# Kernel tuning notes

Measured on AMD Instinct MI355X. Metric: run time of the kernel, lower is better.

Reference implementation:

```python
import jax, jax.numpy as jnp
import numpy as np

N_EMBD = 1024
HEAD_SIZE = 64


def setup_inputs() -> dict:
    key = jax.random.key(0)
    kx, kq, kk, kv = jax.random.split(key, 4)
    B, T = 8, 2048
    x = jax.random.normal(kx, (B, T, N_EMBD), dtype=jnp.float32)
    s = 1.0 / np.sqrt(N_EMBD)
    Wq = jax.random.normal(kq, (N_EMBD, HEAD_SIZE), dtype=jnp.float32) * s
    Wk = jax.random.normal(kk, (N_EMBD, HEAD_SIZE), dtype=jnp.float32) * s
    Wv = jax.random.normal(kv, (N_EMBD, HEAD_SIZE), dtype=jnp.float32) * s
    return {"x": x, "Wq": Wq, "Wk": Wk, "Wv": Wv}


def reference(x, Wq, Wk, Wv):
    # x: [B, T, C]; W*: [C, H]
    q = jnp.einsum('btc,ch->bth', x, Wq)
    k = jnp.einsum('btc,ch->bth', x, Wk)
    v = jnp.einsum('btc,ch->bth', x, Wv)
    H = q.shape[-1]
    score = jnp.einsum('bth,bsh->bts', q, k) / jnp.sqrt(jnp.asarray(H, q.dtype))
    T = score.shape[-1]
    causal = jnp.tril(jnp.ones((T, T), dtype=bool))  # [T, T]
    score = jnp.where(causal, score, -jnp.inf)
    attn = jax.nn.softmax(score, axis=-1)
    return jnp.einsum('bts,bsh->bth', attn, v)
```

## Files before the change

kernel.cpp:

```cpp
#include <hip/hip_runtime.h>

typedef __bf16 bf16;
typedef __attribute__((ext_vector_type(8))) __bf16 bf16x8;
typedef __attribute__((ext_vector_type(4))) __bf16 bf16x4;
typedef __attribute__((ext_vector_type(4))) float floatx4;

#define MFMA16(a, b, c) __builtin_amdgcn_mfma_f32_16x16x32_bf16((a), (b), (c), 0, 0, 0)

__global__ void prep_w(const float* __restrict__ Wq, const float* __restrict__ Wk,
                       const float* __restrict__ Wv, bf16* __restrict__ wTf) {
    int tid = blockIdx.x * 256 + threadIdx.x;
    int j = tid & 7;
    int l = (tid >> 3) & 15;
    int q = (tid >> 7) & 3;
    int kc = (tid >> 9) & 31;
    int mt = tid >> 14;
    int mat = mt >> 2;
    int h = ((mt & 3) << 4) + l;
    int c = kc * 32 + q * 8 + j;
    const float* W = (mat == 0) ? Wq : (mat == 1) ? Wk : Wv;
    wTf[tid] = (bf16)W[c * 64 + h];
}

__global__ __launch_bounds__(256, 2) void proj_qkv(const float* __restrict__ x,
                                                   const bf16* __restrict__ wTf,
                                                   bf16* __restrict__ q,
                                                   bf16* __restrict__ k,
                                                   bf16* __restrict__ vT) {
    __shared__ __align__(16) char xsb[32 * 2048];

    const int tid = threadIdx.x;
    const int lane = tid & 63;
    const int w = tid >> 6;
    const int l15 = lane & 15;
    const int quad = lane >> 4;
    const int T0 = blockIdx.x * 32;

    const int r = tid >> 4;
    const int cm = tid & 15;
    const float* g0 = x + (size_t)(T0 + r) * 1024 + cm * 8;
    const float* g1 = x + (size_t)(T0 + r + 16) * 1024 + cm * 8;
    char* ld0 = xsb + r * 2048;
    char* ld1 = xsb + (r + 16) * 2048;
    const int sws = (r & 7) << 4;

#define STC8(ldb, c, f0, f1)                                                    \
    {                                                                            \
        bf16x8 pk;                                                               \
        pk[0] = (bf16)(f0)[0]; pk[1] = (bf16)(f0)[1];                            \
        pk[2] = (bf16)(f0)[2]; pk[3] = (bf16)(f0)[3];                            \
        pk[4] = (bf16)(f1)[0]; pk[5] = (bf16)(f1)[1];                            \
        pk[6] = (bf16)(f1)[2]; pk[7] = (bf16)(f1)[3];                            \
        *(bf16x8*)((ldb) + ((cm * 16 + (c) * 256) ^ sws)) = pk;                  \
    }

    floatx4 fA[8], fB[8], hA[8], hB[8];
    #pragma unroll
    for (int c = 0; c < 4; c++) {
        fA[2*c]   = *(const floatx4*)(g0 + c * 128);
        fA[2*c+1] = *(const floatx4*)(g0 + c * 128 + 4);
        fB[2*c]   = *(const floatx4*)(g1 + c * 128);
        fB[2*c+1] = *(const floatx4*)(g1 + c * 128 + 4);
    }
    #pragma unroll
    for (int c = 0; c < 4; c++) {
        hA[2*c]   = *(const floatx4*)(g0 + 512 + c * 128);
        hA[2*c+1] = *(const floatx4*)(g0 + 512 + c * 128 + 4);
        hB[2*c]   = *(const floatx4*)(g1 + 512 + c * 128);
        hB[2*c+1] = *(const floatx4*)(g1 + 512 + c * 128 + 4);
    }
    #pragma unroll
    for (int c = 0; c < 4; c++) {
        STC8(ld0, c, fA[2*c], fA[2*c+1]);
        STC8(ld1, c, fB[2*c], fB[2*c+1]);
    }
    __syncthreads();

    floatx4 acc[6] = {};
    const bf16* aw0 = wTf + (size_t)(w * 3 + 0) * 16384 + lane * 8;
    const bf16* aw1 = wTf + (size_t)(w * 3 + 1) * 16384 + lane * 8;
    const bf16* aw2 = wTf + (size_t)(w * 3 + 2) * 16384 + lane * 8;
    const char* xr = xsb + l15 * 2048;
    const int sx = (l15 & 7) << 4;
    const int q16 = quad * 16;

    bf16x8 a0c = *(const bf16x8*)(aw0);
    bf16x8 a1c = *(const bf16x8*)(aw1);
    bf16x8 a2c = *(const bf16x8*)(aw2);
    bf16x8 a0n = *(const bf16x8*)(aw0 + 512);
    bf16x8 a1n = *(const bf16x8*)(aw1 + 512);
    bf16x8 a2n = *(const bf16x8*)(aw2 + 512);

#define KBODY(kc)                                                               \
    {                                                                            \
        bf16x8 p0 = *(const bf16x8*)(aw0 + ((kc) + 2) * 512);                    \
        bf16x8 p1 = *(const bf16x8*)(aw1 + ((kc) + 2) * 512);                    \
        bf16x8 p2 = *(const bf16x8*)(aw2 + ((kc) + 2) * 512);                    \
        const int o = ((kc) * 64 + q16) ^ sx;                                    \
        bf16x8 b0 = *(const bf16x8*)(xr + o);                                    \
        bf16x8 b1 = *(const bf16x8*)(xr + 32768 + o);                            \
        acc[0] = MFMA16(a0c, b0, acc[0]);                                        \
        acc[1] = MFMA16(a0c, b1, acc[1]);                                        \
        acc[2] = MFMA16(a1c, b0, acc[2]);                                        \
        acc[3] = MFMA16(a1c, b1, acc[3]);                                        \
        acc[4] = MFMA16(a2c, b0, acc[4]);                                        \
        acc[5] = MFMA16(a2c, b1, acc[5]);                                        \
        a0c = a0n; a1c = a1n; a2c = a2n;                                         \
        a0n = p0;  a1n = p1;  a2n = p2;                                          \
    }

    #pragma unroll 4
    for (int kc = 0; kc < 16; kc++) KBODY(kc);

    #pragma unroll
    for (int c = 4; c < 8; c++) {
        STC8(ld0, c, hA[2*(c-4)], hA[2*(c-4)+1]);
        STC8(ld1, c, hB[2*(c-4)], hB[2*(c-4)+1]);
    }
    __syncthreads();

    #pragma unroll 4
    for (int kc = 16; kc < 32; kc++) KBODY(kc);
#undef KBODY
#undef STC8

    #pragma unroll
    for (int i = 0; i < 3; i++) {
        int mtile = w * 3 + i;
        int mat = mtile >> 2;
        int hbase = ((mtile & 3) << 4) + (quad << 2);
        float sc = (mat == 0) ? 0.18033688011112042f : 1.0f;
        #pragma unroll
        for (int tt = 0; tt < 2; tt++) {
            const int t = T0 + tt * 16 + l15;
            floatx4 av = acc[i * 2 + tt];
            bf16x4 pk;
            pk[0] = (bf16)(av[0] * sc);
            pk[1] = (bf16)(av[1] * sc);
            pk[2] = (bf16)(av[2] * sc);
            pk[3] = (bf16)(av[3] * sc);
            if (mat == 0) {
                *(bf16x4*)(q + (size_t)t * 64 + hbase) = pk;
            } else if (mat == 1) {
                *(bf16x4*)(k + (size_t)t * 64 + hbase) = pk;
            } else {
                int bidx = t >> 11, tmod = t & 2047;
                #pragma unroll
                for (int rr = 0; rr < 4; rr++)
                    vT[(size_t)(bidx * 64 + hbase + rr) * 2048 + tmod] = pk[rr];
            }
        }
    }
}

#define KP2 72
#define OH 68

__global__ __launch_bounds__(512, 4) void flash(const bf16* __restrict__ q,
                                                const bf16* __restrict__ k,
                                                const bf16* __restrict__ vT,
                                                float* __restrict__ out) {
    __shared__ char smem[8 * 16 * OH * 4];
    __shared__ float Ms[8][16], Ls[8][16];
    bf16* psall = (bf16*)smem;
    float* Os = (float*)smem;

    const int b = blockIdx.x & 7;
    const int p = blockIdx.x >> 3;
    const int t0A = p * 16;
    const int t0B = (127 - p) * 16;
    const int nttA = (p >> 2) + 1;
    const int nttB = ((127 - p) >> 2) + 1;
    const int L = nttA + nttB;

    const int tid = threadIdx.x;
    const int w = tid >> 6;
    const int lane = tid & 63;
    const int l15 = lane & 15;
    const int quad = lane >> 4;

    const int s0 = (L * w) >> 3;
    const int s1 = (L * (w + 1)) >> 3;

    const bf16* kbase = k + (size_t)(b * 2048 + l15) * 64 + quad * 8;
    const bf16* vbase = vT + (size_t)(b * 64 + l15) * 2048 + quad * 8;
    bf16* psw = psall + w * 16 * KP2;

    const bf16* qpA = q + (size_t)(b * 2048 + t0A + l15) * 64 + quad * 8;
    const bf16* qpB = q + (size_t)(b * 2048 + t0B + l15) * 64 + quad * 8;

    floatx4 oA[4] = {}, oB[4] = {};
    float miA = -1e30f, liA = 0.f, miB = -1e30f, liB = 0.f;

#define KV_STEP(jtv, isdiag, t0v, qf0v, qf1v, mi_, li_, o_)                          \
    {                                                                                 \
        const bf16* kp = kbase + (size_t)(jtv) * 4096;                                \
        floatx4 stt[4];                                                               \
        __builtin_amdgcn_s_setprio(1);                                                \
        _Pragma("unroll") for (int mt = 0; mt < 4; mt++) {                            \
            floatx4 z = {};                                                           \
            bf16x8 ka0 = *(const bf16x8*)(kp + mt * 1024);                            \
            bf16x8 ka1 = *(const bf16x8*)(kp + mt * 1024 + 32);                       \
            z = MFMA16(ka0, qf0v, z);                                                 \
            z = MFMA16(ka1, qf1v, z);                                                 \
            stt[mt] = z;                                                              \
        }                                                                             \
        __builtin_amdgcn_s_setprio(0);                                                \
        if (isdiag) {                                                                 \
            _Pragma("unroll") for (int mt = 0; mt < 4; mt++)                          \
                _Pragma("unroll") for (int rr = 0; rr < 4; rr++) {                    \
                    int kv = (jtv) * 64 + mt * 16 + quad * 4 + rr;                    \
                    if (kv > (t0v) + l15) stt[mt][rr] = -1e30f;                       \
                }                                                                     \
        }                                                                             \
        float m0_ = fmaxf(fmaxf(stt[0][0], stt[0][1]), stt[0][2]);                    \
        float m1_ = fmaxf(fmaxf(stt[0][3], stt[1][0]), stt[1][1]);                    \
        float m2_ = fmaxf(fmaxf(stt[1][2], stt[1][3]), stt[2][0]);                    \
        float m3_ = fmaxf(fmaxf(stt[2][1], stt[2][2]), stt[2][3]);                    \
        float m4_ = fmaxf(fmaxf(stt[3][0], stt[3][1]), stt[3][2]);                    \
        float mx = fmaxf(fmaxf(fmaxf(m0_, m1_), m2_),                                 \
                         fmaxf(fmaxf(m3_, m4_), stt[3][3]));                          \
        mx = fmaxf(mx, __shfl_xor(mx, 16, 64));                                       \
        mx = fmaxf(mx, __shfl_xor(mx, 32, 64));                                       \
        const bool nodefer = !__all(mx - mi_ <= 8.0f);                                \
        const float mnew = nodefer ? fmaxf(mi_, mx) : mi_;                            \
        float rs = 0.f;                                                               \
        _Pragma("unroll") for (int mt = 0; mt < 4; mt++)                              \
            _Pragma("unroll") for (int rr = 0; rr < 4; rr++) {                        \
                float pv = __builtin_amdgcn_exp2f(stt[mt][rr] - mnew);                \
                stt[mt][rr] = pv;                                                     \
                rs += pv;                                                             \
            }                                                                         \
        rs += __shfl_xor(rs, 16, 64);                                                 \
        rs += __shfl_xor(rs, 32, 64);                                                 \
        if (nodefer) {                                                                \
            const float aa = __builtin_amdgcn_exp2f(mi_ - mnew);                      \
            mi_ = mnew;                                                               \
            li_ *= aa;                                                                \
            _Pragma("unroll") for (int mt = 0; mt < 4; mt++)                          \
                _Pragma("unroll") for (int rr = 0; rr < 4; rr++) o_[mt][rr] *= aa;    \
        }                                                                             \
        li_ += rs;                                                                    \
        _Pragma("unroll") for (int mt = 0; mt < 4; mt++) {                            \
            bf16x4 pk;                                                                \
            pk[0] = (bf16)stt[mt][0]; pk[1] = (bf16)stt[mt][1];                       \
            pk[2] = (bf16)stt[mt][2]; pk[3] = (bf16)stt[mt][3];                       \
            *(bf16x4*)(psw + l15 * KP2 + mt * 16 + quad * 4) = pk;                    \
        }                                                                             \
        const bf16* vp = vbase + (jtv) * 64;                                          \
        __builtin_amdgcn_s_setprio(1);                                                \
        _Pragma("unroll") for (int kc = 0; kc < 2; kc++) {                            \
            bf16x8 pb = *(const bf16x8*)(psw + l15 * KP2 + kc * 32 + quad * 8);       \
            _Pragma("unroll") for (int mt = 0; mt < 4; mt++) {                        \
                bf16x8 va = *(const bf16x8*)(vp + mt * 32768 + kc * 32);              \
                o_[mt] = MFMA16(va, pb, o_[mt]);                                      \
            }                                                                         \
        }                                                                             \
        __builtin_amdgcn_s_setprio(0);                                                \
    }

    {
        const int eA = (s1 < nttA) ? s1 : nttA;
        if (s0 < eA) {
            bf16x8 qf0 = *(const bf16x8*)qpA;
            bf16x8 qf1 = *(const bf16x8*)(qpA + 32);
            for (int s = s0; s < eA; s++) {
                KV_STEP(s, (s == nttA - 1), t0A, qf0, qf1, miA, liA, oA);
            }
        }
    }
    {
        const int sB = (s0 > nttA) ? s0 : nttA;
        if (sB < s1) {
            bf16x8 qf0 = *(const bf16x8*)qpB;
            bf16x8 qf1 = *(const bf16x8*)(qpB + 32);
            for (int s = sB; s < s1; s++) {
                KV_STEP(s - nttA, (s == L - 1), t0B, qf0, qf1, miB, liB, oB);
            }
        }
    }

    #pragma unroll
    for (int tile = 0; tile < 2; tile++) {
        __syncthreads();
        float mi = tile ? miB : miA;
        float li = tile ? liB : liA;
        if (lane < 16) { Ms[w][lane] = mi; Ls[w][lane] = li; }
        #pragma unroll
        for (int mt = 0; mt < 4; mt++) {
            floatx4 ov = tile ? oB[mt] : oA[mt];
            *(floatx4*)(Os + (w * 16 + l15) * OH + mt * 16 + quad * 4) = ov;
        }
        __syncthreads();
        {
            int qq = tid >> 5;
            int h2 = (tid & 31) * 2;
            float Mg = -1e30f;
            #pragma unroll
            for (int u = 0; u < 8; u++) Mg = fmaxf(Mg, Ms[u][qq]);
            float Lg = 0.f, v0 = 0.f, v1 = 0.f;
            #pragma unroll
            for (int u = 0; u < 8; u++) {
                float sw = __builtin_amdgcn_exp2f(Ms[u][qq] - Mg);
                Lg += sw * Ls[u][qq];
                const float* Or = Os + (u * 16 + qq) * OH + h2;
                v0 += sw * Or[0];
                v1 += sw * Or[1];
            }
            float inv = 1.0f / Lg;
            int t0v = tile ? t0B : t0A;
            float* op = out + (size_t)(b * 2048 + t0v + qq) * 64 + h2;
            op[0] = v0 * inv;
            op[1] = v1 * inv;
        }
    }
#undef KV_STEP
}

extern "C" void kernel_launch(void* const* d_in, const int* in_sizes, int n_in,
                              void* d_out, int out_size, void* d_ws, size_t ws_size,
                              hipStream_t stream) {
    const float* x  = (const float*)d_in[0];
    const float* Wq = (const float*)d_in[1];
    const float* Wk = (const float*)d_in[2];
    const float* Wv = (const float*)d_in[3];
    float* out = (float*)d_out;

    char* ws = (char*)d_ws;
    bf16* wTf = (bf16*)ws;
    bf16* q   = (bf16*)(ws + 397312);
    bf16* k   = (bf16*)(ws + 397312 + 2097152);
    bf16* vT  = (bf16*)(ws + 397312 + 2 * 2097152);

    hipLaunchKernelGGL(prep_w,   dim3(768), dim3(256), 0, stream, Wq, Wk, Wv, wTf);
    hipLaunchKernelGGL(proj_qkv, dim3(512), dim3(256), 0, stream, x, wTf, q, k, vT);
    hipLaunchKernelGGL(flash,    dim3(512), dim3(512), 0, stream, q, k, vT, out);
}
```

Baseline: 140.5 us.

## Process two query tiles per KV step in flash kernel to reuse K/V loads

Each flash block now handles four 16-row query tiles (two near, two far) instead of two. Each wave loads a K and V tile once and feeds it to two query tiles, which halves K/V global loads per unit of work. The grid drops to 256 blocks and launch bounds drop to 2 blocks per SM to make room for the extra registers and shared memory. Costs are higher register pressure, fewer blocks to hide latency, and coarser load balancing, since the diagonal mask now covers two tiles that share the same KV range.

```diff
diff --git a/kernel.cpp b/kernel.cpp
--- a/kernel.cpp
+++ b/kernel.cpp
@@ -155,23 +155,26 @@
 
 #define KP2 72
 #define OH 68
-
-__global__ __launch_bounds__(512, 4) void flash(const bf16* __restrict__ q,
+#define PSB (16 * KP2)
+
+__global__ __launch_bounds__(512, 2) void flash(const bf16* __restrict__ q,
                                                 const bf16* __restrict__ k,
                                                 const bf16* __restrict__ vT,
                                                 float* __restrict__ out) {
-    __shared__ char smem[8 * 16 * OH * 4];
+    __shared__ char smem[36864];
     __shared__ float Ms[8][16], Ls[8][16];
     bf16* psall = (bf16*)smem;
     float* Os = (float*)smem;
 
     const int b = blockIdx.x & 7;
-    const int p = blockIdx.x >> 3;
-    const int t0A = p * 16;
-    const int t0B = (127 - p) * 16;
-    const int nttA = (p >> 2) + 1;
-    const int nttB = ((127 - p) >> 2) + 1;
-    const int L = nttA + nttB;
+    const int j = blockIdx.x >> 3;
+    const int Tn0 = 32 * j;
+    const int Tn1 = Tn0 + 16;
+    const int Tf0 = (126 - 2 * j) * 16;
+    const int Tf1 = Tf0 + 16;
+    const int NN = (j >> 1) + 1;
+    const int NF = ((63 - j) >> 1) + 1;
+    const int L = NN + NF;
 
     const int tid = threadIdx.x;
     const int w = tid >> 6;
@@ -179,116 +182,155 @@
     const int l15 = lane & 15;
     const int quad = lane >> 4;
 
-    const int s0 = (L * w) >> 3;
-    const int s1 = (L * (w + 1)) >> 3;
+    const int u0 = (L * w) >> 3;
+    const int u1 = (L * (w + 1)) >> 3;
 
     const bf16* kbase = k + (size_t)(b * 2048 + l15) * 64 + quad * 8;
     const bf16* vbase = vT + (size_t)(b * 64 + l15) * 2048 + quad * 8;
-    bf16* psw = psall + w * 16 * KP2;
-
-    const bf16* qpA = q + (size_t)(b * 2048 + t0A + l15) * 64 + quad * 8;
-    const bf16* qpB = q + (size_t)(b * 2048 + t0B + l15) * 64 + quad * 8;
-
-    floatx4 oA[4] = {}, oB[4] = {};
-    float miA = -1e30f, liA = 0.f, miB = -1e30f, liB = 0.f;
-
-#define KV_STEP(jtv, isdiag, t0v, qf0v, qf1v, mi_, li_, o_)                          \
+    bf16* pswa = psall + w * 2 * PSB;
+    bf16* pswb = pswa + PSB;
+
+    const bf16* qn0 = q + (size_t)(b * 2048 + Tn0 + l15) * 64 + quad * 8;
+    const bf16* qn1 = q + (size_t)(b * 2048 + Tn1 + l15) * 64 + quad * 8;
+    const bf16* qx0 = q + (size_t)(b * 2048 + Tf0 + l15) * 64 + quad * 8;
+    const bf16* qx1 = q + (size_t)(b * 2048 + Tf1 + l15) * 64 + quad * 8;
+
+    floatx4 o0[4] = {}, o1[4] = {}, o2[4] = {}, o3[4] = {};
+    float mm0 = -1e30f, ll0 = 0.f, mm1 = -1e30f, ll1 = 0.f;
+    float mm2 = -1e30f, ll2 = 0.f, mm3 = -1e30f, ll3 = 0.f;
+
+#define SMPART(mi_, li_, o_, pswX)                                                   \
     {                                                                                 \
-        const bf16* kp = kbase + (size_t)(jtv) * 4096;                                \
+        float x0_ = fmaxf(fmaxf(stt[0][0], stt[0][1]), stt[0][2]);                    \
+        float x1_ = fmaxf(fmaxf(stt[0][3], stt[1][0]), stt[1][1]);                    \
+        float x2_ = fmaxf(fmaxf(stt[1][2], stt[1][3]), stt[2][0]);                    \
+        float x3_ = fmaxf(fmaxf(stt[2][1], stt[2][2]), stt[2][3]);                    \
+        float x4_ = fmaxf(fmaxf(stt[3][0], stt[3][1]), stt[3][2]);                    \
+        float mx_ = fmaxf(fmaxf(fmaxf(x0_, x1_), x2_),                                \
+                          fmaxf(fmaxf(x3_, x4_), stt[3][3]));                         \
+        mx_ = fmaxf(mx_, __shfl_xor(mx_, 16, 64));                                    \
+        mx_ = fmaxf(mx_, __shfl_xor(mx_, 32, 64));                                    \
+        const bool nd_ = !__all(mx_ - mi_ <= 8.0f);                                   \
+        const float mn_ = nd_ ? fmaxf(mi_, mx_) : mi_;                                \
+        float rs_ = 0.f;                                                              \
+        _Pragma("unroll") for (int mt_ = 0; mt_ < 4; mt_++)                           \
+            _Pragma("unroll") for (int rr_ = 0; rr_ < 4; rr_++) {                     \
+                float pv_ = __builtin_amdgcn_exp2f(stt[mt_][rr_] - mn_);              \
+                stt[mt_][rr_] = pv_;                                                  \
+                rs_ += pv_;                                                           \
+            }                                                                         \
+        rs_ += __shfl_xor(rs_, 16, 64);                                               \
+        rs_ += __shfl_xor(rs_, 32, 64);                                               \
+        if (nd_) {                                                                    \
+            const float aa_ = __builtin_amdgcn_exp2f(mi_ - mn_);                      \
+            mi_ = mn_;                                                                \
+            li_ *= aa_;                                                               \
+            _Pragma("unroll") for (int mt_ = 0; mt_ < 4; mt_++)                       \
+                _Pragma("unroll") for (int rr_ = 0; rr_ < 4; rr_++) o_[mt_][rr_] *= aa_; \
+        }                                                                             \
+        li_ += rs_;                                                                   \
+        _Pragma("unroll") for (int mt_ = 0; mt_ < 4; mt_++) {                         \
+            bf16x4 pk_;                                                               \
+            pk_[0] = (bf16)stt[mt_][0]; pk_[1] = (bf16)stt[mt_][1];                   \
+            pk_[2] = (bf16)stt[mt_][2]; pk_[3] = (bf16)stt[mt_][3];                   \
+            *(bf16x4*)((pswX) + l15 * KP2 + mt_ * 16 + quad * 4) = pk_;               \
+        }                                                                             \
+    }
+
+#define KV_STEP2(jtv, isdiag, T0a_, T0b_, qa0_, qa1_, qb0_, qb1_,                     \
+                 m_a, l_a, o_a, m_b, l_b, o_b)                                        \
+    {                                                                                 \
+        const bf16* kp_ = kbase + (size_t)(jtv) * 4096;                               \
+        bf16x8 kv0_ = *(const bf16x8*)(kp_);                                          \
+        bf16x8 kv1_ = *(const bf16x8*)(kp_ + 32);                                     \
+        bf16x8 kv2_ = *(const bf16x8*)(kp_ + 1024);                                   \
+        bf16x8 kv3_ = *(const bf16x8*)(kp_ + 1024 + 32);                              \
+        bf16x8 kv4_ = *(const bf16x8*)(kp_ + 2048);                                   \
+        bf16x8 kv5_ = *(const bf16x8*)(kp_ + 2048 + 32);                              \
+        bf16x8 kv6_ = *(const bf16x8*)(kp_ + 3072);                                   \
+        bf16x8 kv7_ = *(const bf16x8*)(kp_ + 3072 + 32);                              \
         floatx4 stt[4];                                                               \
         __builtin_amdgcn_s_setprio(1);                                                \
-        _Pragma("unroll") for (int mt = 0; mt < 4; mt++) {                            \
-            floatx4 z = {};                                                           \
-            bf16x8 ka0 = *(const bf16x8*)(kp + mt * 1024);                            \
-            bf16x8 ka1 = *(const bf16x8*)(kp + mt * 1024 + 32);                       \
-            z = MFMA16(ka0, qf0v, z);                                                 \
-            z = MFMA16(ka1, qf1v, z);                                                 \
-            stt[mt] = z;                                                              \
-        }                                                                             \
+        { floatx4 z_ = {}; z_ = MFMA16(kv0_, qa0_, z_); z_ = MFMA16(kv1_, qa1_, z_); stt[0] = z_; } \
+        { floatx4 z_ = {}; z_ = MFMA16(kv2_, qa0_, z_); z_ = MFMA16(kv3_, qa1_, z_); stt[1] = z_; } \
+        { floatx4 z_ = {}; z_ = MFMA16(kv4_, qa0_, z_); z_ = MFMA16(kv5_, qa1_, z_); stt[2] = z_; } \
+        { floatx4 z_ = {}; z_ = MFMA16(kv6_, qa0_, z_); z_ = MFMA16(kv7_, qa1_, z_); stt[3] = z_; } \
         __builtin_amdgcn_s_setprio(0);                                                \
         if (isdiag) {                                                                 \
-            _Pragma("unroll") for (int mt = 0; mt < 4; mt++)                          \
-                _Pragma("unroll") for (int rr = 0; rr < 4; rr++) {                    \
-                    int kv = (jtv) * 64 + mt * 16 + quad * 4 + rr;                    \
-                    if (kv > (t0v) + l15) stt[mt][rr] = -1e30f;                       \
+            _Pragma("unroll") for (int mt_ = 0; mt_ < 4; mt_++)                       \
+                _Pragma("unroll") for (int rr_ = 0; rr_ < 4; rr_++) {                 \
+                    int kv_ = (jtv) * 64 + mt_ * 16 + quad * 4 + rr_;                 \
+                    if (kv_ > (T0a_) + l15) stt[mt_][rr_] = -1e30f;                   \
                 }                                                                     \
         }                                                                             \
-        float m0_ = fmaxf(fmaxf(stt[0][0], stt[0][1]), stt[0][2]);                    \
-        float m1_ = fmaxf(fmaxf(stt[0][3], stt[1][0]), stt[1][1]);                    \
-        float m2_ = fmaxf(fmaxf(stt[1][2], stt[1][3]), stt[2][0]);                    \
-        float m3_ = fmaxf(fmaxf(stt[2][1], stt[2][2]), stt[2][3]);                    \
-        float m4_ = fmaxf(fmaxf(stt[3][0], stt[3][1]), stt[3][2]);                    \
-        float mx = fmaxf(fmaxf(fmaxf(m0_, m1_), m2_),                                 \
-                         fmaxf(fmaxf(m3_, m4_), stt[3][3]));                          \
-        mx = fmaxf(mx, __shfl_xor(mx, 16, 64));                                       \
-        mx = fmaxf(mx, __shfl_xor(mx, 32, 64));                                       \
-        const bool nodefer = !__all(mx - mi_ <= 8.0f);                                \
-        const float mnew = nodefer ? fmaxf(mi_, mx) : mi_;                            \
-        float rs = 0.f;                                                               \
-        _Pragma("unroll") for (int mt = 0; mt < 4; mt++)                              \
-            _Pragma("unroll") for (int rr = 0; rr < 4; rr++) {                        \
-                float pv = __builtin_amdgcn_exp2f(stt[mt][rr] - mnew);                \
-                stt[mt][rr] = pv;                                                     \
-                rs += pv;                                                             \
-            }                                                                         \
-        rs += __shfl_xor(rs, 16, 64);                                                 \
-        rs += __shfl_xor(rs, 32, 64);                                                 \
-        if (nodefer) {                                                                \
-            const float aa = __builtin_amdgcn_exp2f(mi_ - mnew);                      \
-            mi_ = mnew;                                                               \
-            li_ *= aa;                                                                \
-            _Pragma("unroll") for (int mt = 0; mt < 4; mt++)                          \
-                _Pragma("unroll") for (int rr = 0; rr < 4; rr++) o_[mt][rr] *= aa;    \
-        }                                                                             \
-        li_ += rs;                                                                    \
-        _Pragma("unroll") for (int mt = 0; mt < 4; mt++) {                            \
-            bf16x4 pk;                                                                \
-            pk[0] = (bf16)stt[mt][0]; pk[1] = (bf16)stt[mt][1];                       \
-            pk[2] = (bf16)stt[mt][2]; pk[3] = (bf16)stt[mt][3];                       \
-            *(bf16x4*)(psw + l15 * KP2 + mt * 16 + quad * 4) = pk;                    \
-        }                                                                             \
-        const bf16* vp = vbase + (jtv) * 64;                                          \
+        SMPART(m_a, l_a, o_a, pswa);                                                  \
         __builtin_amdgcn_s_setprio(1);                                                \
-        _Pragma("unroll") for (int kc = 0; kc < 2; kc++) {                            \
-            bf16x8 pb = *(const bf16x8*)(psw + l15 * KP2 + kc * 32 + quad * 8);       \
-            _Pragma("unroll") for (int mt = 0; mt < 4; mt++) {                        \
-                bf16x8 va = *(const bf16x8*)(vp + mt * 32768 + kc * 32);              \
-                o_[mt] = MFMA16(va, pb, o_[mt]);                                      \
-            }                                                                         \
-        }                                                                             \
+        { floatx4 z_ = {}; z_ = MFMA16(kv0_, qb0_, z_); z_ = MFMA16(kv1_, qb1_, z_); stt[0] = z_; } \
+        { floatx4 z_ = {}; z_ = MFMA16(kv2_, qb0_, z_); z_ = MFMA16(kv3_, qb1_, z_); stt[1] = z_; } \
+        { floatx4 z_ = {}; z_ = MFMA16(kv4_, qb0_, z_); z_ = MFMA16(kv5_, qb1_, z_); stt[2] = z_; } \
+        { floatx4 z_ = {}; z_ = MFMA16(kv6_, qb0_, z_); z_ = MFMA16(kv7_, qb1_, z_); stt[3] = z_; } \
         __builtin_amdgcn_s_setprio(0);                                                \
+        if (isdiag) {                                                                 \
+            _Pragma("unroll") for (int mt_ = 0; mt_ < 4; mt_++)                       \
+                _Pragma("unroll") for (int rr_ = 0; rr_ < 4; rr_++) {                 \
+                    int kv_ = (jtv) * 64 + mt_ * 16 + quad * 4 + rr_;                 \
+                    if (kv_ > (T0b_) + l15) stt[mt_][rr_] = -1e30f;                   \
+                }                                                                     \
+        }                                                                             \
+        SMPART(m_b, l_b, o_b, pswb);                                                  \
+        const bf16* vp_ = vbase + (size_t)(jtv) * 64;                                 \
+        bf16x8 pa0_ = *(const bf16x8*)(pswa + l15 * KP2 + quad * 8);                  \
+        bf16x8 pa1_ = *(const bf16x8*)(pswa + l15 * KP2 + 32 + quad * 8);             \
+        bf16x8 pb0_ = *(const bf16x8*)(pswb + l15 * KP2 + quad * 8);                  \
+        bf16x8 pb1_ = *(const bf16x8*)(pswb + l15 * KP2 + 32 + quad * 8);             \
+        __builtin_amdgcn_s_setprio(1);                                                \
+        _Pragma("unroll") for (int mt_ = 0; mt_ < 4; mt_++) {                         \
+            bf16x8 v0_ = *(const bf16x8*)(vp_ + mt_ * 32768);                         \
+            bf16x8 v1_ = *(const bf16x8*)(vp_ + mt_ * 32768 + 32);                    \
+            o_a[mt_] = MFMA16(v0_, pa0_, o_a[mt_]);                                   \
+            o_a[mt_] = MFMA16(v1_, pa1_, o_a[mt_]);                                   \
+            o_b[mt_] = MFMA16(v0_, pb0_, o_b[mt_]);                                   \
+            o_b[mt_] = MFMA16(v1_, pb1_, o_b[mt_]);                                   \
+        }                                                                             \
+        __builtin_amdgcn_s_setprio(0);                                                \
     }
 
     {
-        const int eA = (s1 < nttA) ? s1 : nttA;
-        if (s0 < eA) {
-            bf16x8 qf0 = *(const bf16x8*)qpA;
-            bf16x8 qf1 = *(const bf16x8*)(qpA + 32);
-            for (int s = s0; s < eA; s++) {
-                KV_STEP(s, (s == nttA - 1), t0A, qf0, qf1, miA, liA, oA);
+        const int e = (u1 < NN) ? u1 : NN;
+        if (u0 < e) {
+            bf16x8 qa0 = *(const bf16x8*)qn0;
+            bf16x8 qa1 = *(const bf16x8*)(qn0 + 32);
+            bf16x8 qb0 = *(const bf16x8*)qn1;
+            bf16x8 qb1 = *(const bf16x8*)(qn1 + 32);
+            for (int s = u0; s < e; s++) {
+                KV_STEP2(s, (s == NN - 1), Tn0, Tn1, qa0, qa1, qb0, qb1,
+                         mm0, ll0, o0, mm1, ll1, o1);
             }
         }
     }
     {
-        const int sB = (s0 > nttA) ? s0 : nttA;
-        if (sB < s1) {
-            bf16x8 qf0 = *(const bf16x8*)qpB;
-            bf16x8 qf1 = *(const bf16x8*)(qpB + 32);
-            for (int s = sB; s < s1; s++) {
-                KV_STEP(s - nttA, (s == L - 1), t0B, qf0, qf1, miB, liB, oB);
+        const int sB = (u0 > NN) ? u0 : NN;
+        if (sB < u1) {
+            bf16x8 qa0 = *(const bf16x8*)qx0;
+            bf16x8 qa1 = *(const bf16x8*)(qx0 + 32);
+            bf16x8 qb0 = *(const bf16x8*)qx1;
+            bf16x8 qb1 = *(const bf16x8*)(qx1 + 32);
+            for (int s = sB; s < u1; s++) {
+                KV_STEP2(s - NN, (s == L - 1), Tf0, Tf1, qa0, qa1, qb0, qb1,
+                         mm2, ll2, o2, mm3, ll3, o3);
             }
         }
     }
 
     #pragma unroll
-    for (int tile = 0; tile < 2; tile++) {
+    for (int r = 0; r < 4; r++) {
         __syncthreads();
-        float mi = tile ? miB : miA;
-        float li = tile ? liB : liA;
+        float mi = (r == 0) ? mm0 : (r == 1) ? mm1 : (r == 2) ? mm2 : mm3;
+        float li = (r == 0) ? ll0 : (r == 1) ? ll1 : (r == 2) ? ll2 : ll3;
         if (lane < 16) { Ms[w][lane] = mi; Ls[w][lane] = li; }
         #pragma unroll
         for (int mt = 0; mt < 4; mt++) {
-            floatx4 ov = tile ? oB[mt] : oA[mt];
+            floatx4 ov = (r == 0) ? o0[mt] : (r == 1) ? o1[mt] : (r == 2) ? o2[mt] : o3[mt];
             *(floatx4*)(Os + (w * 16 + l15) * OH + mt * 16 + quad * 4) = ov;
         }
         __syncthreads();
@@ -308,13 +350,14 @@
                 v1 += sw * Or[1];
             }
             float inv = 1.0f / Lg;
-            int t0v = tile ? t0B : t0A;
-            float* op = out + (size_t)(b * 2048 + t0v + qq) * 64 + h2;
+            int T0v = (r == 0) ? Tn0 : (r == 1) ? Tn1 : (r == 2) ? Tf0 : Tf1;
+            float* op = out + (size_t)(b * 2048 + T0v + qq) * 64 + h2;
             op[0] = v0 * inv;
             op[1] = v1 * inv;
         }
     }
-#undef KV_STEP
+#undef KV_STEP2
+#undef SMPART
 }
 
 extern "C" void kernel_launch(void* const* d_in, const int* in_sizes, int n_in,
@@ -334,5 +377,5 @@
 
     hipLaunchKernelGGL(prep_w,   dim3(768), dim3(256), 0, stream, Wq, Wk, Wv, wTf);
     hipLaunchKernelGGL(proj_qkv, dim3(512), dim3(256), 0, stream, x, wTf, q, k, vT);
-    hipLaunchKernelGGL(flash,    dim3(512), dim3(512), 0, stream, q, k, vT, out);
+    hipLaunchKernelGGL(flash,    dim3(256), dim3(512), 0, stream, q, k, vT, out);
 }
```

After: 128.1 us. -8.8%, faster.
